# Kernel tuning notes

Hardware: AMD Instinct MI355X
Metric: run time of the kernel (lower is better)

Reference implementation:

```python
import jax, jax.numpy as jnp
import numpy as np

# --- fixed OpenCV filter kernels ---
# cv2.getGaussianKernel(3, 1): exp(-(i-1)^2/2), normalized -> [0.27407, 0.45186, 0.27407]
_g = np.exp(-((np.arange(3) - 1.0) ** 2) / 2.0)
GAUSS_1D = (_g / _g.sum()).astype(np.float32)
# cv2 Sobel/Laplacian ksize=9 separable parts (unnormalized, as cv2.Laplacian uses):
#   smoothing = binomial row C(8,k); second derivative = C(6,k) conv [1,-2,1]
SMOOTH_9 = np.array([1, 8, 28, 56, 70, 56, 28, 8, 1], dtype=np.float32)
D2_9 = np.array([1, 4, 4, -4, -10, -4, 4, 4, 1], dtype=np.float32)


def _depthwise_conv(x, k2d):
    """Depthwise 2D correlation with BORDER_REFLECT_101 padding (cv2 default).

    x: [N,H,W,C] float, k2d: [kh,kw] float (symmetric, so corr == conv)."""
    C = x.shape[-1]
    rh, rw = k2d.shape[0] // 2, k2d.shape[1] // 2
    # jnp 'reflect' == OpenCV BORDER_REFLECT_101 (edge pixel not duplicated)
    xp = jnp.pad(x, ((0, 0), (rh, rh), (rw, rw), (0, 0)), mode='reflect')
    k = jnp.broadcast_to(k2d[:, :, None, None], (k2d.shape[0], k2d.shape[1], 1, C))
    return jax.lax.conv_general_dilated(
        xp, k, window_strides=(1, 1), padding='VALID',
        dimension_numbers=('NHWC', 'HWIO', 'NHWC'),
        feature_group_count=C)


def setup_inputs() -> dict:
    key = jax.random.key(0)
    # uint8-range image batch, as the original layer feeds uint8 data to OpenCV
    x = jax.random.uniform(key, (32, 512, 512, 3), dtype=jnp.float32) * 255.0
    return {"x": x}


def reference(x) -> jnp.ndarray:
    g = jnp.asarray(GAUSS_1D)
    blur = _depthwise_conv(x, jnp.outer(g, g))  # GaussianBlur(ksize=3, sigma=1)
    lap_k = jnp.asarray(np.outer(SMOOTH_9, D2_9) + np.outer(D2_9, SMOOTH_9))
    lap = _depthwise_conv(blur, lap_k) + 1.0  # delta = 1
    # CV_8UC1 destination depth -> saturate to [0, 255]
    return jnp.clip(lap, 0.0, 255.0)
```

## Files before the change

kernel.cpp:

```cpp
#include <hip/hip_runtime.h>


#define TH 32
#define TW 32
#define FW (TW*3)
#define BW (TW+8)
#define BF (BW*3)
#define BH (TH+8)
#define XHMAX (TH+10)
#define HIMG 512
#define WIMG 512
#define ROWF (WIMG*3)

#define SM_TOTAL 12480

__device__ __forceinline__ int reflect101(int i, int n) {
    i = (i < 0) ? -i : i;
    return (i >= n) ? (2 * n - 2 - i) : i;
}

__device__ __forceinline__ float4 fma4(float s, const float4& a, const float4& b) {
    return make_float4(fmaf(s, a.x, b.x), fmaf(s, a.y, b.y),
                       fmaf(s, a.z, b.z), fmaf(s, a.w, b.w));
}

__global__ __launch_bounds__(256, 3)
void log_fused(const float* __restrict__ x, float* __restrict__ out) {
    __shared__ __align__(16) float smem[SM_TOTAL];
    __shared__ int brow[BH][3];
    float* const blur  = smem;
    float* const hblur = smem + 4800;
    float* const t1    = smem + 4800;
    float* const t2    = smem + 8640;

    const int tid  = threadIdx.x;
    const int col0 = blockIdx.x * TW;
    const int row0 = blockIdx.y * TH;
    const int n    = blockIdx.z;

    const int R0    = max(0, row0 - 5);
    const int R1    = min(HIMG - 1, row0 + TH + 4);
    const int nrows = R1 - R0 + 1;

    if (tid < BH) {
        int gr = reflect101(row0 - 4 + tid, HIMG);
        brow[tid][0] = reflect101(gr - 1, HIMG) - R0;
        brow[tid][1] = gr - R0;
        brow[tid][2] = reflect101(gr + 1, HIMG) - R0;
    }

    const float G0 = 0.2740686190f, G1 = 0.4518627620f;

    if (tid < 240) {
        const int lc  = tid % BF;
        const int rg  = tid / BF;
        const int lcp = lc / 3;
        const int ch  = lc - 3 * lcp;
        const int gc  = reflect101(col0 - 4 + lcp, WIMG);
        const int xm  = reflect101(gc - 1, WIMG) * 3 + ch;
        const int x0  = gc * 3 + ch;
        const int xp  = reflect101(gc + 1, WIMG) * 3 + ch;
        const float* xr = x + ((size_t)n * HIMG + (size_t)(R0 + rg)) * ROWF;
        for (int r = rg; r < nrows; r += 2, xr += 2 * ROWF) {
            hblur[r * BF + lc] = G0 * (xr[xm] + xr[xp]) + G1 * xr[x0];
        }
    }
    __syncthreads();

    for (int e = tid; e < (BH * BF) / 4; e += 256) {
        int lr = e / (BF / 4);
        int qc = e - lr * (BF / 4);
        int lc = qc * 4;
        const float4 a = *(const float4*)&hblur[brow[lr][0] * BF + lc];
        const float4 b = *(const float4*)&hblur[brow[lr][1] * BF + lc];
        const float4 c = *(const float4*)&hblur[brow[lr][2] * BF + lc];
        float4 r;
        r.x = G0 * (a.x + c.x) + G1 * b.x;
        r.y = G0 * (a.y + c.y) + G1 * b.y;
        r.z = G0 * (a.z + c.z) + G1 * b.z;
        r.w = G0 * (a.w + c.w) + G1 * b.w;
        *(float4*)&blur[lr * BF + lc] = r;
    }
    __syncthreads();

    const float S9[9] = {1.f, 8.f, 28.f, 56.f, 70.f, 56.f, 28.f, 8.f, 1.f};
    const float D9[9] = {1.f, 4.f, 4.f, -4.f, -10.f, -4.f, 4.f, 4.f, 1.f};

    for (int g = tid; g < (TH / 2) * (BF / 4); g += 256) {
        int rg  = g / (BF / 4);
        int qc  = g - rg * (BF / 4);
        int lr0 = rg * 2;
        int lc  = qc * 4;
        float4 w[10];
        #pragma unroll
        for (int k = 0; k < 10; ++k)
            w[k] = *(const float4*)&blur[(lr0 + k) * BF + lc];
        float4 a1r0 = make_float4(0.f, 0.f, 0.f, 0.f), a2r0 = a1r0;
        float4 a1r1 = a1r0, a2r1 = a1r0;
        #pragma unroll
        for (int k = 0; k < 9; ++k) {
            a1r0 = fma4(S9[k], w[k],     a1r0);
            a2r0 = fma4(D9[k], w[k],     a2r0);
            a1r1 = fma4(S9[k], w[k + 1], a1r1);
            a2r1 = fma4(D9[k], w[k + 1], a2r1);
        }
        *(float4*)&t1[(lr0    ) * BF + lc] = a1r0;
        *(float4*)&t1[(lr0 + 1) * BF + lc] = a1r1;
        *(float4*)&t2[(lr0    ) * BF + lc] = a2r0;
        *(float4*)&t2[(lr0 + 1) * BF + lc] = a2r1;
    }
    __syncthreads();

    float* const outn = out + (size_t)n * HIMG * ROWF;
    for (int g = tid; g < TH * (FW / 8); g += 256) {
        int lr = g / (FW / 8);
        int qp = g - lr * (FW / 8);
        int lc = qp * 8;
        float w1[32], w2[32];
        #pragma unroll
        for (int q = 0; q < 8; ++q) {
            float4 v = *(const float4*)&t1[lr * BF + lc + 4 * q];
            w1[4*q+0] = v.x; w1[4*q+1] = v.y; w1[4*q+2] = v.z; w1[4*q+3] = v.w;
            float4 u = *(const float4*)&t2[lr * BF + lc + 4 * q];
            w2[4*q+0] = u.x; w2[4*q+1] = u.y; w2[4*q+2] = u.z; w2[4*q+3] = u.w;
        }
        float o[8];
        #pragma unroll
        for (int j = 0; j < 8; ++j) {
            float a = 1.0f;
            #pragma unroll
            for (int k = 0; k < 9; ++k) {
                a = fmaf(D9[k], w1[j + 3 * k], a);
                a = fmaf(S9[k], w2[j + 3 * k], a);
            }
            o[j] = fminf(fmaxf(a, 0.0f), 255.0f);
        }
        float* op = outn + (size_t)(row0 + lr) * ROWF + (size_t)(col0 * 3 + lc);
        *(float4*)&op[0] = make_float4(o[0], o[1], o[2], o[3]);
        *(float4*)&op[4] = make_float4(o[4], o[5], o[6], o[7]);
    }
}

extern "C" void kernel_launch(void* const* d_in, const int* in_sizes, int n_in,
                              void* d_out, int out_size, void* d_ws, size_t ws_size,
                              hipStream_t stream) {
    const float* x = (const float*)d_in[0];
    float* outp = (float*)d_out;
    const int nimg = in_sizes[0] / (HIMG * WIMG * 3);
    dim3 grid(WIMG / TW, HIMG / TH, nimg);
    log_fused<<<grid, dim3(256, 1, 1), 0, stream>>>(x, outp);
}
```

Before: 251.6 us.

## Halve tile height, fuse separable Gaussian into one pass, pad smem rows

Tile height drops from 32 to 16 rows and occupancy is raised to 5 blocks per CU. The separable Gaussian blur is fused: each thread computes three horizontal blurs straight from global memory and combines them vertically, removing the intermediate hblur buffer, one barrier and the row-index table. The shared row stride is padded to 132 floats and the loops become fixed single-pass thread mappings. The trade-off is more redundant global reads and more halo recomputation per output row, since the 8-row halo is now spread over 16 rows instead of 32.

Result: slower. 264.4 us (+5.1%).

```diff
diff --git a/kernel.cpp b/kernel.cpp
--- a/kernel.cpp
+++ b/kernel.cpp
@@ -1,18 +1,16 @@
 #include <hip/hip_runtime.h>
 
 
-#define TH 32
+#define TH 16
 #define TW 32
 #define FW (TW*3)
-#define BW (TW+8)
-#define BF (BW*3)
-#define BH (TH+8)
-#define XHMAX (TH+10)
+#define BP (TW+8)
+#define BFU (BP*3)
+#define BF 132
+#define BHR (TH+8)
 #define HIMG 512
 #define WIMG 512
 #define ROWF (WIMG*3)
-
-#define SM_TOTAL 12480
 
 __device__ __forceinline__ int reflect101(int i, int n) {
     i = (i < 0) ? -i : i;
@@ -24,73 +22,51 @@
                        fmaf(s, a.z, b.z), fmaf(s, a.w, b.w));
 }
 
-__global__ __launch_bounds__(256, 3)
+__global__ __launch_bounds__(256, 5)
 void log_fused(const float* __restrict__ x, float* __restrict__ out) {
-    __shared__ __align__(16) float smem[SM_TOTAL];
-    __shared__ int brow[BH][3];
-    float* const blur  = smem;
-    float* const hblur = smem + 4800;
-    float* const t1    = smem + 4800;
-    float* const t2    = smem + 8640;
+    __shared__ __align__(16) float blur[BHR * BF];
+    __shared__ __align__(16) float t1[TH * BF];
+    __shared__ __align__(16) float t2[TH * BF];
 
     const int tid  = threadIdx.x;
     const int col0 = blockIdx.x * TW;
     const int row0 = blockIdx.y * TH;
-    const int n    = blockIdx.z;
-
-    const int R0    = max(0, row0 - 5);
-    const int R1    = min(HIMG - 1, row0 + TH + 4);
-    const int nrows = R1 - R0 + 1;
-
-    if (tid < BH) {
-        int gr = reflect101(row0 - 4 + tid, HIMG);
-        brow[tid][0] = reflect101(gr - 1, HIMG) - R0;
-        brow[tid][1] = gr - R0;
-        brow[tid][2] = reflect101(gr + 1, HIMG) - R0;
-    }
+    const float* const xn = x + (size_t)blockIdx.z * HIMG * ROWF;
 
     const float G0 = 0.2740686190f, G1 = 0.4518627620f;
 
     if (tid < 240) {
-        const int lc  = tid % BF;
-        const int rg  = tid / BF;
-        const int lcp = lc / 3;
-        const int ch  = lc - 3 * lcp;
-        const int gc  = reflect101(col0 - 4 + lcp, WIMG);
-        const int xm  = reflect101(gc - 1, WIMG) * 3 + ch;
-        const int x0  = gc * 3 + ch;
-        const int xp  = reflect101(gc + 1, WIMG) * 3 + ch;
-        const float* xr = x + ((size_t)n * HIMG + (size_t)(R0 + rg)) * ROWF;
-        for (int r = rg; r < nrows; r += 2, xr += 2 * ROWF) {
-            hblur[r * BF + lc] = G0 * (xr[xm] + xr[xp]) + G1 * xr[x0];
+        const int lc = tid % BFU;
+        const int rg = tid / BFU;
+        const int p  = lc / 3;
+        const int ch = lc - 3 * p;
+        const int gc = reflect101(col0 - 4 + p, WIMG);
+        const int xm = reflect101(gc - 1, WIMG) * 3 + ch;
+        const int x0 = gc * 3 + ch;
+        const int xp = reflect101(gc + 1, WIMG) * 3 + ch;
+        #pragma unroll
+        for (int r = rg; r < BHR; r += 2) {
+            const int g  = row0 - 4 + r;
+            const int gr = reflect101(g, HIMG);
+            const float* pa = xn + (size_t)reflect101(gr - 1, HIMG) * ROWF;
+            const float* pb = xn + (size_t)gr * ROWF;
+            const float* pc = xn + (size_t)reflect101(gr + 1, HIMG) * ROWF;
+            const float h0 = G0 * (pa[xm] + pa[xp]) + G1 * pa[x0];
+            const float h1 = G0 * (pb[xm] + pb[xp]) + G1 * pb[x0];
+            const float h2 = G0 * (pc[xm] + pc[xp]) + G1 * pc[x0];
+            blur[r * BF + lc] = G0 * (h0 + h2) + G1 * h1;
         }
-    }
-    __syncthreads();
-
-    for (int e = tid; e < (BH * BF) / 4; e += 256) {
-        int lr = e / (BF / 4);
-        int qc = e - lr * (BF / 4);
-        int lc = qc * 4;
-        const float4 a = *(const float4*)&hblur[brow[lr][0] * BF + lc];
-        const float4 b = *(const float4*)&hblur[brow[lr][1] * BF + lc];
-        const float4 c = *(const float4*)&hblur[brow[lr][2] * BF + lc];
-        float4 r;
-        r.x = G0 * (a.x + c.x) + G1 * b.x;
-        r.y = G0 * (a.y + c.y) + G1 * b.y;
-        r.z = G0 * (a.z + c.z) + G1 * b.z;
-        r.w = G0 * (a.w + c.w) + G1 * b.w;
-        *(float4*)&blur[lr * BF + lc] = r;
     }
     __syncthreads();
 
     const float S9[9] = {1.f, 8.f, 28.f, 56.f, 70.f, 56.f, 28.f, 8.f, 1.f};
     const float D9[9] = {1.f, 4.f, 4.f, -4.f, -10.f, -4.f, 4.f, 4.f, 1.f};
 
-    for (int g = tid; g < (TH / 2) * (BF / 4); g += 256) {
-        int rg  = g / (BF / 4);
-        int qc  = g - rg * (BF / 4);
-        int lr0 = rg * 2;
-        int lc  = qc * 4;
+    if (tid < 240) {
+        const int rg  = tid / 30;
+        const int qc  = tid - rg * 30;
+        const int lr0 = rg * 2;
+        const int lc  = qc * 4;
         float4 w[10];
         #pragma unroll
         for (int k = 0; k < 10; ++k)
@@ -111,11 +87,10 @@
     }
     __syncthreads();
 
-    float* const outn = out + (size_t)n * HIMG * ROWF;
-    for (int g = tid; g < TH * (FW / 8); g += 256) {
-        int lr = g / (FW / 8);
-        int qp = g - lr * (FW / 8);
-        int lc = qp * 8;
+    if (tid < 192) {
+        const int lr = tid / 12;
+        const int qp = tid - lr * 12;
+        const int lc = qp * 8;
         float w1[32], w2[32];
         #pragma unroll
         for (int q = 0; q < 8; ++q) {
@@ -135,7 +110,8 @@
             }
             o[j] = fminf(fmaxf(a, 0.0f), 255.0f);
         }
-        float* op = outn + (size_t)(row0 + lr) * ROWF + (size_t)(col0 * 3 + lc);
+        float* op = out + (size_t)blockIdx.z * HIMG * ROWF
+                        + (size_t)(row0 + lr) * ROWF + (size_t)(col0 * 3 + lc);
         *(float4*)&op[0] = make_float4(o[0], o[1], o[2], o[3]);
         *(float4*)&op[4] = make_float4(o[4], o[5], o[6], o[7]);
     }
```
